# Performance work log

Measured on AMD Instinct MI355X. Metric: run time of the kernel, lower is better.

Reference implementation:

```python
import jax, jax.numpy as jnp
import numpy as np
from jax import lax

B, T, S, F = 16, 32, 128, 3
H = 256          # encoder_hidden = decoder_hidden = decoder_input
NH = 8           # n_head
TP = 4           # t_predict
DK = H // NH


def _lin(k, fan_in, shape):
    return jax.random.normal(k, shape, jnp.float32) * (1.0 / np.sqrt(fan_in))


def setup_inputs() -> dict:
    key = jax.random.key(0)
    ks = jax.random.split(key, 14)
    return {
        "input_data": jax.random.normal(ks[0], (B, T, S, F), jnp.float32),
        # encoder attention-LSTM cell (input_size=3)
        "enc_Wq": _lin(ks[1], H, (H, H)),
        "enc_Wk": _lin(ks[2], H, (H, H)),
        "enc_Wv": _lin(ks[3], H, (H, H)),
        "enc_Wg": _lin(ks[4], F + 2 * H, (F + 2 * H, 4 * H)),
        "enc_bg": jnp.zeros((4 * H,), jnp.float32),
        # decoder attention-LSTM cell (input_size=decoder_input=H)
        "dec_Wq": _lin(ks[5], H, (H, H)),
        "dec_Wk": _lin(ks[6], H, (H, H)),
        "dec_Wv": _lin(ks[7], H, (H, H)),
        "dec_Wg": _lin(ks[8], 3 * H, (3 * H, 4 * H)),
        "dec_bg": jnp.zeros((4 * H,), jnp.float32),
        # embedding Linear(encoder_hidden -> decoder_input)
        "emb_W": _lin(ks[9], H, (H, H)),
        "emb_b": jnp.zeros((H,), jnp.float32),
        # output Linear(decoder_hidden -> output_size=1)
        "out_W": _lin(ks[10], H, (H, 1)),
        "out_b": jnp.zeros((1,), jnp.float32),
    }


def spatial_hidden(h):
    # h: [B,S,H] -> [B,S,4,H] neighbors at offsets (+2,+1,-1,-2), zero-padded
    z1 = jnp.zeros_like(h[:, :1])
    z2 = jnp.zeros_like(h[:, :2])
    after1 = jnp.concatenate([h[:, 1:], z1], axis=1)
    before1 = jnp.concatenate([z1, h[:, :-1]], axis=1)
    after2 = jnp.concatenate([h[:, 2:], z2], axis=1)
    before2 = jnp.concatenate([z2, h[:, :-2]], axis=1)
    return jnp.stack([after2, after1, before1, before2], axis=2)


def attn_lstm_cell(x, h, c, sp, Wq, Wk, Wv, Wg, bg):
    # x:[B,S,Fin] h,c:[B,S,H] sp:[B,S,4,H]
    b, s, _ = h.shape
    q = (h @ Wq).reshape(b, s, NH, DK)
    k = (sp @ Wk).reshape(b, s, 4, NH, DK)
    v = (sp @ Wv).reshape(b, s, 4, NH, DK)
    scores = jnp.einsum('bshd,bsnhd->bshn', q, k) / np.sqrt(DK).astype(np.float32)
    attn = jax.nn.softmax(scores, axis=-1)
    ctx = jnp.einsum('bshn,bsnhd->bshd', attn, v).reshape(b, s, H)
    z = jnp.concatenate([x, h, ctx], axis=-1) @ Wg + bg
    i, f, g, o = jnp.split(z, 4, axis=-1)
    c_new = jax.nn.sigmoid(f) * c + jax.nn.sigmoid(i) * jnp.tanh(g)
    h_new = jax.nn.sigmoid(o) * jnp.tanh(c_new)
    return h_new, c_new


def reference(input_data, enc_Wq, enc_Wk, enc_Wv, enc_Wg, enc_bg,
              dec_Wq, dec_Wk, dec_Wv, dec_Wg, dec_bg,
              emb_W, emb_b, out_W, out_b):
    b, t, s, f = input_data.shape
    eh = jnp.zeros((b, s, H), input_data.dtype)
    ec = jnp.zeros((b, s, H), input_data.dtype)
    dh = jnp.zeros((b, s, H), input_data.dtype)

    cur = jnp.swapaxes(input_data[:, :-1], 0, 1)  # [T-1,B,S,F]
    nxt = jnp.swapaxes(input_data[:, 1:], 0, 1)   # [T-1,B,S,F]

    def step(carry, xt):
        eh, ec, dh = carry
        x_cur, x_nxt = xt
        esp = spatial_hidden(eh)
        dsp = spatial_hidden(dh)
        eh, ec = attn_lstm_cell(x_cur, eh, ec, esp, enc_Wq, enc_Wk, enc_Wv, enc_Wg, enc_bg)
        code = jax.nn.sigmoid(eh @ emb_W + emb_b)
        # NOTE: original code passes decoder_h as both h and c (decoder_c unused)
        dh, _ = attn_lstm_cell(code, dh, dh, dsp, dec_Wq, dec_Wk, dec_Wv, dec_Wg, dec_bg)
        out = dh @ out_W + out_b                                   # [B,S,1]
        In = jnp.concatenate([x_nxt[:, 0:1, 1:2], out[:, :-1, :]], axis=1)
        num = x_cur[:, :, 2:3] + In - out
        next_data = jnp.concatenate([out, In, num], axis=2)        # [B,S,3]
        return (eh, ec, dh), next_data

    _, outs = lax.scan(step, (eh, ec, dh), (cur, nxt))
    # keep only steps with time >= t_predict
    return jnp.swapaxes(outs[TP:], 0, 1)  # [B, T-TP-1, S, 3]
```

## Files before the change

kernel.cpp:

```cpp
#include <hip/hip_runtime.h>
#include <hip/hip_bf16.h>

#define Bz 16
#define Tz 32
#define Sz 128
#define TPz 4
#define Mz (Bz*Sz)
#define NSTEP (Tz-1)

typedef __bf16 bf16x8 __attribute__((ext_vector_type(8)));
typedef float  f32x4  __attribute__((ext_vector_type(4)));

#define MFMA __builtin_amdgcn_mfma_f32_16x16x32_bf16

__device__ __forceinline__ float sigf(float x) { return 1.f/(1.f + __expf(-x)); }

__global__ __launch_bounds__(256) void prep3(
    const float* __restrict__ encWq, const float* __restrict__ encWk,
    const float* __restrict__ encWv, const float* __restrict__ encWg,
    const float* __restrict__ decWq, const float* __restrict__ decWk,
    const float* __restrict__ decWv, const float* __restrict__ decWg,
    const float* __restrict__ embW,
    __bf16* __restrict__ Pqkv_e, __bf16* __restrict__ Pqkv_d,
    __bf16* __restrict__ Pemb,   __bf16* __restrict__ Pg_e,
    __bf16* __restrict__ Pg_d)
{
    int id = blockIdx.x * 256 + threadIdx.x;
    if (id < 768*256) {
        int f = id >> 9, e = id & 511, l = e >> 3, j = e & 7;
        int nt = f >> 3, kt = f & 7;
        int n = nt*16 + (l & 15), k = kt*32 + (l >> 4)*8 + j;
        float v = (n < 256) ? encWq[k*256 + n]
                : (n < 512) ? encWk[k*256 + (n-256)]
                            : encWv[k*256 + (n-512)];
        Pqkv_e[id] = (__bf16)v; return;
    }
    id -= 768*256;
    if (id < 768*256) {
        int f = id >> 9, e = id & 511, l = e >> 3, j = e & 7;
        int nt = f >> 3, kt = f & 7;
        int n = nt*16 + (l & 15), k = kt*32 + (l >> 4)*8 + j;
        float v = (n < 256) ? decWq[k*256 + n]
                : (n < 512) ? decWk[k*256 + (n-256)]
                            : decWv[k*256 + (n-512)];
        Pqkv_d[id] = (__bf16)v; return;
    }
    id -= 768*256;
    if (id < 256*256) {
        int f = id >> 9, e = id & 511, l = e >> 3, j = e & 7;
        int nt = f >> 3, kt = f & 7;
        int n = nt*16 + (l & 15), k = kt*32 + (l >> 4)*8 + j;
        Pemb[id] = (__bf16)embW[k*256 + n]; return;
    }
    id -= 256*256;
    if (id < 1024*512) {
        int f = id >> 9, e = id & 511, l = e >> 3, j = e & 7;
        int nt = f >> 4, kt = f & 15;
        int cht = nt >> 2, g = nt & 3;
        int ch = cht*16 + (l & 15), k = kt*32 + (l >> 4)*8 + j;
        Pg_e[id] = (__bf16)encWg[(size_t)(3 + k)*1024 + g*256 + ch]; return;
    }
    id -= 1024*512;
    if (id < 1024*768) {
        int f = id >> 9, e = id & 511, l = e >> 3, j = e & 7;
        int nt = f / 24, kt = f % 24;
        int cht = nt >> 2, g = nt & 3;
        int ch = cht*16 + (l & 15), k = kt*32 + (l >> 4)*8 + j;
        Pg_d[id] = (__bf16)decWg[(size_t)k*1024 + g*256 + ch]; return;
    }
}

__device__ __forceinline__ void qkv_lds(
    const __bf16* src264, const __bf16* __restrict__ P,
    __bf16* qL, __bf16* kvL, int tid)
{
    const int w = tid >> 6, lane = tid & 63, quad = (lane >> 4), lr = lane & 15;
    #pragma unroll
    for (int ng = 0; ng < 3; ++ng) {
        const int ntA = w*6 + ng*2;
        f32x4 acc[2][3];
        #pragma unroll
        for (int i = 0; i < 2; ++i)
            #pragma unroll
            for (int m = 0; m < 3; ++m) acc[i][m] = f32x4{0.f,0.f,0.f,0.f};
        for (int kt = 0; kt < 8; ++kt) {
            bf16x8 a0 = *(const bf16x8*)&src264[(lr)*264      + kt*32 + quad*8];
            bf16x8 a1 = *(const bf16x8*)&src264[(16 + lr)*264 + kt*32 + quad*8];
            bf16x8 a2 = *(const bf16x8*)&src264[(32 + lr)*264 + kt*32 + quad*8];
            bf16x8 b0 = *(const bf16x8*)&P[((size_t)(ntA*8 + kt)*64 + lane)*8];
            bf16x8 b1 = *(const bf16x8*)&P[((size_t)((ntA+1)*8 + kt)*64 + lane)*8];
            acc[0][0] = MFMA(a0, b0, acc[0][0], 0,0,0);
            acc[0][1] = MFMA(a1, b0, acc[0][1], 0,0,0);
            acc[0][2] = MFMA(a2, b0, acc[0][2], 0,0,0);
            acc[1][0] = MFMA(a0, b1, acc[1][0], 0,0,0);
            acc[1][1] = MFMA(a1, b1, acc[1][1], 0,0,0);
            acc[1][2] = MFMA(a2, b1, acc[1][2], 0,0,0);
        }
        #pragma unroll
        for (int i = 0; i < 2; ++i) {
            const int col = (ntA + i)*16 + lr;
            #pragma unroll
            for (int m = 0; m < 3; ++m)
                #pragma unroll
                for (int r = 0; r < 4; ++r) {
                    const int row = m*16 + quad*4 + r;
                    const float v = acc[i][m][r];
                    if (col < 256) {
                        if (row >= 2 && row < 34) qL[(row-2)*264 + col] = (__bf16)v;
                    } else if (row < 36) {
                        kvL[row*520 + (col - 256)] = (__bf16)v;
                    }
                }
        }
    }
}

__device__ __forceinline__ void attn_lds(
    const __bf16* qL, const __bf16* kvL, __bf16* cxL, int s0, int tid)
{
    const int w = tid >> 6, lane = tid & 63, quad = lane >> 4, lr = lane & 15;
    const int r = 4*w + quad, s = s0 + r, ch0 = lr*16;

    float q[16];
    {
        bf16x8 q0 = *(const bf16x8*)&qL[r*264 + ch0];
        bf16x8 q1 = *(const bf16x8*)&qL[r*264 + ch0 + 8];
        #pragma unroll
        for (int i = 0; i < 8; ++i) { q[i] = (float)q0[i]; q[8+i] = (float)q1[i]; }
    }
    bf16x8 zv;
    #pragma unroll
    for (int i = 0; i < 8; ++i) zv[i] = (__bf16)0.f;

    const int offs[4] = {2, 1, -1, -2};
    float sc[4]; bf16x8 v0[4], v1[4];
    #pragma unroll
    for (int n = 0; n < 4; ++n) {
        const int s2 = s + offs[n];
        const bool ok = ((unsigned)s2 < 128u);
        const int lrow = r + offs[n] + 2;
        float p = 0.f;
        if (ok) {
            bf16x8 k0 = *(const bf16x8*)&kvL[lrow*520 + ch0];
            bf16x8 k1 = *(const bf16x8*)&kvL[lrow*520 + ch0 + 8];
            v0[n] = *(const bf16x8*)&kvL[lrow*520 + 256 + ch0];
            v1[n] = *(const bf16x8*)&kvL[lrow*520 + 256 + ch0 + 8];
            #pragma unroll
            for (int i = 0; i < 8; ++i) p += q[i]*(float)k0[i] + q[8+i]*(float)k1[i];
        } else { v0[n] = zv; v1[n] = zv; }
        p += __shfl_xor(p, 1);
        sc[n] = ok ? p * 0.17677669529663687f : 0.f;
    }
    const float mx = fmaxf(fmaxf(sc[0], sc[1]), fmaxf(sc[2], sc[3]));
    float se = 0.f, aw[4];
    #pragma unroll
    for (int n = 0; n < 4; ++n) { aw[n] = __expf(sc[n] - mx); se += aw[n]; }
    const float inv = 1.f / se;
    float cx[16];
    #pragma unroll
    for (int i = 0; i < 16; ++i) cx[i] = 0.f;
    #pragma unroll
    for (int n = 0; n < 4; ++n)
        #pragma unroll
        for (int i = 0; i < 8; ++i) {
            cx[i]   += aw[n]*(float)v0[n][i];
            cx[8+i] += aw[n]*(float)v1[n][i];
        }
    bf16x8 o0, o1;
    #pragma unroll
    for (int i = 0; i < 8; ++i) { o0[i] = (__bf16)(cx[i]*inv); o1[i] = (__bf16)(cx[8+i]*inv); }
    *(bf16x8*)&cxL[r*264 + ch0]     = o0;
    *(bf16x8*)&cxL[r*264 + ch0 + 8] = o1;
}

#define SM_A264   0
#define SM_R      19008
#define SM_CODE   35904
#define SM_Q      56448
#define SM_MISC   73344
#define SM_TOTAL  73856

__global__ __launch_bounds__(512, 4) void step_k(
    int k, const float* __restrict__ input,
    __bf16* __restrict__ P, __bf16* __restrict__ Q,
    const __bf16* __restrict__ Pqkv_e, const __bf16* __restrict__ Pqkv_d,
    const __bf16* __restrict__ Pemb,   const __bf16* __restrict__ Pg_e,
    const __bf16* __restrict__ Pg_d,
    const float* __restrict__ encWg, const float* __restrict__ encbg,
    const float* __restrict__ decbg, const float* __restrict__ embb,
    const float* __restrict__ outW,
    float* __restrict__ ec, float* __restrict__ outbuf)
{
    __shared__ __attribute__((aligned(16))) char SM[SM_TOTAL];

    const int tid  = threadIdx.x;
    const int w    = tid >> 6;
    const int lane = tid & 63;
    const int quad = lane >> 4, lr = lane & 15;
    const int mt = w >> 2, ct = w & 3;

    __bf16* aL  = (__bf16*)(SM + SM_A264);
    __bf16* kvL = (__bf16*)(SM + SM_R);
    __bf16* qL  = (__bf16*)(SM + SM_Q);
    __bf16* cxL = qL;

    if (blockIdx.x >= 256) {
        if (k >= NSTEP) return;
        const int bid = blockIdx.x - 256;
        const int b = bid >> 4, rg = (bid >> 2) & 3, qt = bid & 3;
        const int gbatch = b*128, s0 = rg*32, grow0 = gbatch + s0;
        const int ch = qt*64 + ct*16 + lr;
        float* xL = (float*)(SM + SM_MISC);

        for (int v = tid; v < 36*32; v += 512) {
            const int row = v >> 5, seg = v & 31, s = s0 - 2 + row;
            bf16x8 val;
            if ((unsigned)s < 128u)
                val = *(const bf16x8*)&P[(size_t)(gbatch + s)*512 + seg*8];
            else {
                #pragma unroll
                for (int i = 0; i < 8; ++i) val[i] = (__bf16)0.f;
            }
            *(bf16x8*)&aL[row*264 + seg*8] = val;
        }
        if (tid < 96) xL[tid] = input[((size_t)(b*Tz + k)*Sz + s0)*3 + tid];
        __syncthreads();

        qkv_lds(aL, Pqkv_e, qL, kvL, tid);
        __syncthreads();
        attn_lds(qL, kvL, cxL, s0, tid);
        __syncthreads();

        float wx0[4], wx1[4], wx2[4], bgv[4];
        #pragma unroll
        for (int g = 0; g < 4; ++g) {
            const int c = g*256 + ch;
            wx0[g] = encWg[c]; wx1[g] = encWg[1024 + c]; wx2[g] = encWg[2048 + c];
            bgv[g] = encbg[c];
        }
        f32x4 acc[4];
        #pragma unroll
        for (int g = 0; g < 4; ++g) acc[g] = f32x4{0.f,0.f,0.f,0.f};
        for (int kt = 0; kt < 16; ++kt) {
            const __bf16* As = (kt < 8)
                ? &aL [(2 + mt*16 + lr)*264 + kt*32 + quad*8]
                : &cxL[(mt*16 + lr)*264 + (kt-8)*32 + quad*8];
            bf16x8 af = *(const bf16x8*)As;
            #pragma unroll
            for (int g = 0; g < 4; ++g) {
                const int nt = qt*16 + ct*4 + g;
                bf16x8 bf = *(const bf16x8*)&Pg_e[((size_t)(nt*16 + kt)*64 + lane)*8];
                acc[g] = MFMA(af, bf, acc[g], 0,0,0);
            }
        }
        #pragma unroll
        for (int r = 0; r < 4; ++r) {
            const int row = mt*16 + quad*4 + r;
            const float x0 = xL[row*3], x1 = xL[row*3+1], x2 = xL[row*3+2];
            const float zi = acc[0][r] + x0*wx0[0] + x1*wx1[0] + x2*wx2[0] + bgv[0];
            const float zf = acc[1][r] + x0*wx0[1] + x1*wx1[1] + x2*wx2[1] + bgv[1];
            const float zg = acc[2][r] + x0*wx0[2] + x1*wx1[2] + x2*wx2[2] + bgv[2];
            const float zo = acc[3][r] + x0*wx0[3] + x1*wx1[3] + x2*wx2[3] + bgv[3];
            const size_t ei = (size_t)(grow0 + row)*256 + ch;
            const float cn = sigf(zf)*ec[ei] + sigf(zi)*tanhf(zg);
            ec[ei] = cn;
            Q[(size_t)(grow0 + row)*512 + ch] = (__bf16)(sigf(zo)*tanhf(cn));
        }
    } else {
        if (k < 1) return;
        const int td = k - 1;
        const int bid = blockIdx.x;
        const int b = bid >> 4, rg = (bid >> 2) & 3, qt = bid & 3;
        const int gbatch = b*128, s0 = rg*32, grow0 = gbatch + s0;
        const int ch = qt*64 + ct*16 + lr;
        __bf16* dhL   = aL;
        __bf16* ehtL  = (__bf16*)(SM + SM_R);
        __bf16* codeL = (__bf16*)(SM + SM_CODE);
        float* outredL = (float*)(SM + SM_MISC);

        for (int v = tid; v < 32*32; v += 512) {
            const int row = v >> 5, seg = v & 31;
            *(bf16x8*)&ehtL[row*264 + seg*8] =
                *(const bf16x8*)&P[(size_t)(grow0 + row)*512 + seg*8];
        }
        for (int v = tid; v < 36*32; v += 512) {
            const int row = v >> 5, seg = v & 31, s = s0 - 2 + row;
            bf16x8 val;
            if ((unsigned)s < 128u)
                val = *(const bf16x8*)&Q[(size_t)(gbatch + s)*512 + 256 + seg*8];
            else {
                #pragma unroll
                for (int i = 0; i < 8; ++i) val[i] = (__bf16)0.f;
            }
            *(bf16x8*)&dhL[row*264 + seg*8] = val;
        }
        __syncthreads();

        {
            f32x4 cacc[2][2];
            #pragma unroll
            for (int m = 0; m < 2; ++m)
                #pragma unroll
                for (int i = 0; i < 2; ++i) cacc[m][i] = f32x4{0.f,0.f,0.f,0.f};
            for (int kt = 0; kt < 8; ++kt) {
                bf16x8 a0 = *(const bf16x8*)&ehtL[(lr)*264      + kt*32 + quad*8];
                bf16x8 a1 = *(const bf16x8*)&ehtL[(16 + lr)*264 + kt*32 + quad*8];
                #pragma unroll
                for (int i = 0; i < 2; ++i) {
                    bf16x8 bf = *(const bf16x8*)&Pemb[((size_t)((2*w + i)*8 + kt)*64 + lane)*8];
                    cacc[0][i] = MFMA(a0, bf, cacc[0][i], 0,0,0);
                    cacc[1][i] = MFMA(a1, bf, cacc[1][i], 0,0,0);
                }
            }
            __syncthreads();
            #pragma unroll
            for (int i = 0; i < 2; ++i) {
                const int col = (2*w + i)*16 + lr;
                const float bb = embb[col];
                #pragma unroll
                for (int m = 0; m < 2; ++m)
                    #pragma unroll
                    for (int r = 0; r < 4; ++r)
                        codeL[(m*16 + quad*4 + r)*264 + col] = (__bf16)sigf(cacc[m][i][r] + bb);
            }
        }
        __syncthreads();

        float bgv[4];
        #pragma unroll
        for (int g = 0; g < 4; ++g) bgv[g] = decbg[g*256 + ch];
        const float ow = outW[ch];

        f32x4 acc[4];
        #pragma unroll
        for (int g = 0; g < 4; ++g) acc[g] = f32x4{0.f,0.f,0.f,0.f};
        for (int kt = 0; kt < 8; ++kt) {
            bf16x8 af = *(const bf16x8*)&codeL[(mt*16 + lr)*264 + kt*32 + quad*8];
            #pragma unroll
            for (int g = 0; g < 4; ++g) {
                const int nt = qt*16 + ct*4 + g;
                bf16x8 bf = *(const bf16x8*)&Pg_d[((size_t)(nt*24 + kt)*64 + lane)*8];
                acc[g] = MFMA(af, bf, acc[g], 0,0,0);
            }
        }
        __syncthreads();

        qkv_lds(dhL, Pqkv_d, qL, kvL, tid);
        __syncthreads();
        attn_lds(qL, kvL, cxL, s0, tid);
        __syncthreads();

        for (int kt = 8; kt < 24; ++kt) {
            const __bf16* As = (kt < 16)
                ? &dhL[(2 + mt*16 + lr)*264 + (kt-8)*32 + quad*8]
                : &cxL[(mt*16 + lr)*264 + (kt-16)*32 + quad*8];
            bf16x8 af = *(const bf16x8*)As;
            #pragma unroll
            for (int g = 0; g < 4; ++g) {
                const int nt = qt*16 + ct*4 + g;
                bf16x8 bf = *(const bf16x8*)&Pg_d[((size_t)(nt*24 + kt)*64 + lane)*8];
                acc[g] = MFMA(af, bf, acc[g], 0,0,0);
            }
        }
        #pragma unroll
        for (int r = 0; r < 4; ++r) {
            const int row = mt*16 + quad*4 + r;
            const float zi = acc[0][r] + bgv[0];
            const float zf = acc[1][r] + bgv[1];
            const float zg = acc[2][r] + bgv[2];
            const float zo = acc[3][r] + bgv[3];
            const float c_old = (float)dhL[(2 + row)*264 + ch];
            const float cn = sigf(zf)*c_old + sigf(zi)*tanhf(zg);
            const float h  = sigf(zo)*tanhf(cn);
            P[(size_t)(grow0 + row)*512 + 256 + ch] = (__bf16)h;
            float pv = h * ow;
            pv += __shfl_xor(pv, 1); pv += __shfl_xor(pv, 2);
            pv += __shfl_xor(pv, 4); pv += __shfl_xor(pv, 8);
            if (lr == 0) outredL[row*4 + ct] = pv;
        }
        __syncthreads();
        if (tid < 32) {
            const float s4 = outredL[tid*4] + outredL[tid*4+1]
                           + outredL[tid*4+2] + outredL[tid*4+3];
            atomicAdd(&outbuf[(size_t)td*Mz + grow0 + tid], s4);
        }
    }
}

__global__ __launch_bounds__(256) void assemble_k(
    const float* __restrict__ outbuf, const float* __restrict__ input,
    const float* __restrict__ outb, float* __restrict__ out)
{
    const int idx = blockIdx.x*256 + threadIdx.x;
    const int NT = NSTEP - TPz;
    if (idx >= Bz*NT*Sz) return;
    const int s  = idx & 127;
    const int bi = idx >> 7;
    const int i  = bi % NT;
    const int b  = bi / NT;
    const int t  = i + TPz;
    const float ob = outb[0];
    const float o  = outbuf[t*Mz + (b<<7) + s] + ob;
    const float In = (s == 0)
        ? input[((size_t)(b*Tz + t + 1)*Sz)*3 + 1]
        : outbuf[t*Mz + (b<<7) + s - 1] + ob;
    const float num = input[((size_t)(b*Tz + t)*Sz + s)*3 + 2] + In - o;
    const size_t base = ((size_t)(b*NT + i)*Sz + s)*3;
    out[base+0] = o;
    out[base+1] = In;
    out[base+2] = num;
}

extern "C" void kernel_launch(void* const* d_in, const int* in_sizes, int n_in,
                              void* d_out, int out_size, void* d_ws, size_t ws_size,
                              hipStream_t stream)
{
    const float* input = (const float*)d_in[0];
    const float* encWq = (const float*)d_in[1];
    const float* encWk = (const float*)d_in[2];
    const float* encWv = (const float*)d_in[3];
    const float* encWg = (const float*)d_in[4];
    const float* encbg = (const float*)d_in[5];
    const float* decWq = (const float*)d_in[6];
    const float* decWk = (const float*)d_in[7];
    const float* decWv = (const float*)d_in[8];
    const float* decWg = (const float*)d_in[9];
    const float* decbg = (const float*)d_in[10];
    const float* embW  = (const float*)d_in[11];
    const float* embb  = (const float*)d_in[12];
    const float* outW  = (const float*)d_in[13];
    const float* outb  = (const float*)d_in[14];

    char* ws = (char*)d_ws;
    size_t off = 0;
    auto alloc = [&](size_t bytes) -> void* {
        void* p = ws + off;
        off += (bytes + 255) & ~(size_t)255;
        return p;
    };
    __bf16* Pqkv_e = (__bf16*)alloc((size_t)768*256*2);
    __bf16* Pqkv_d = (__bf16*)alloc((size_t)768*256*2);
    __bf16* Pemb   = (__bf16*)alloc((size_t)256*256*2);
    __bf16* Pg_e   = (__bf16*)alloc((size_t)1024*512*2);
    __bf16* Pg_d   = (__bf16*)alloc((size_t)1024*768*2);
    __bf16* Xa     = (__bf16*)alloc((size_t)Mz*512*2);
    __bf16* Xb     = (__bf16*)alloc((size_t)Mz*512*2);
    float*  ec     = (float*) alloc((size_t)Mz*256*4);
    float*  outbuf = (float*) alloc((size_t)NSTEP*Mz*4);

    hipMemsetAsync(Xa, 0, (size_t)Mz*512*2, stream);
    hipMemsetAsync(ec, 0, (size_t)Mz*256*4, stream);
    hipMemsetAsync(outbuf, 0, (size_t)NSTEP*Mz*4, stream);

    prep3<<<6912, 256, 0, stream>>>(encWq, encWk, encWv, encWg,
                                    decWq, decWk, decWv, decWg, embW,
                                    Pqkv_e, Pqkv_d, Pemb, Pg_e, Pg_d);

    for (int k = 0; k <= NSTEP; ++k) {
        __bf16* P = (k & 1) ? Xb : Xa;
        __bf16* Q = (k & 1) ? Xa : Xb;
        step_k<<<512, 512, 0, stream>>>(k, input, P, Q,
                                        Pqkv_e, Pqkv_d, Pemb, Pg_e, Pg_d,
                                        encWg, encbg, decbg, embb, outW,
                                        ec, outbuf);
    }
    assemble_k<<<(Bz*(NSTEP-TPz)*Sz + 255)/256, 256, 0, stream>>>(
        outbuf, input, outb, (float*)d_out);
}
```

Baseline: 1.276 ms.

## Fuse per-step launches into a persistent kernel with neighbor progress flags

Replaces the 32 per-timestep kernel launches with one persistent kernel in which each block loops over all steps. Blocks wait on atomic progress counters of only the neighboring encoder and decoder tiles they depend on, instead of a full grid-wide launch boundary. State reads use relaxed agent-scope atomic loads so that fresh data is seen. It removes launch overhead and global barriers, but it depends on all 512 blocks being co-resident and adds spin-wait cost, with a guard that could silently break on timeout.

Result: slower. 5.094 ms (+299.2%).

```diff
diff --git a/kernel.cpp b/kernel.cpp
--- a/kernel.cpp
+++ b/kernel.cpp
@@ -14,6 +14,15 @@
 #define MFMA __builtin_amdgcn_mfma_f32_16x16x32_bf16
 
 __device__ __forceinline__ float sigf(float x) { return 1.f/(1.f + __expf(-x)); }
+
+__device__ __forceinline__ bf16x8 ld_state16(const __bf16* p) {
+    unsigned long long* q = (unsigned long long*)p;
+    unsigned long long lo = __hip_atomic_load(q,     __ATOMIC_RELAXED, __HIP_MEMORY_SCOPE_AGENT);
+    unsigned long long hi = __hip_atomic_load(q + 1, __ATOMIC_RELAXED, __HIP_MEMORY_SCOPE_AGENT);
+    union { unsigned long long u[2]; bf16x8 v; } x;
+    x.u[0] = lo; x.u[1] = hi;
+    return x.v;
+}
 
 __global__ __launch_bounds__(256) void prep3(
     const float* __restrict__ encWq, const float* __restrict__ encWk,
@@ -180,16 +189,17 @@
 #define SM_MISC   73344
 #define SM_TOTAL  73856
 
-__global__ __launch_bounds__(512, 4) void step_k(
-    int k, const float* __restrict__ input,
-    __bf16* __restrict__ P, __bf16* __restrict__ Q,
+__global__ __launch_bounds__(512, 4) void fused_scan(
+    const float* __restrict__ input,
+    __bf16* __restrict__ Xa, __bf16* __restrict__ Xb,
     const __bf16* __restrict__ Pqkv_e, const __bf16* __restrict__ Pqkv_d,
     const __bf16* __restrict__ Pemb,   const __bf16* __restrict__ Pg_e,
     const __bf16* __restrict__ Pg_d,
     const float* __restrict__ encWg, const float* __restrict__ encbg,
     const float* __restrict__ decbg, const float* __restrict__ embb,
     const float* __restrict__ outW,
-    float* __restrict__ ec, float* __restrict__ outbuf)
+    float* __restrict__ ec, float* __restrict__ outbuf,
+    int* __restrict__ encProg, int* __restrict__ decProg)
 {
     __shared__ __attribute__((aligned(16))) char SM[SM_TOTAL];
 
@@ -199,191 +209,232 @@
     const int quad = lane >> 4, lr = lane & 15;
     const int mt = w >> 2, ct = w & 3;
 
+    const bool isEnc = (blockIdx.x >= 256);
+    const int bid = isEnc ? ((int)blockIdx.x - 256) : (int)blockIdx.x;
+    const int b = bid >> 4, rg = (bid >> 2) & 3, qt = bid & 3;
+    const int gbatch = b*128, s0 = rg*32, grow0 = gbatch + s0;
+    const int ch = qt*64 + ct*16 + lr;
+
     __bf16* aL  = (__bf16*)(SM + SM_A264);
     __bf16* kvL = (__bf16*)(SM + SM_R);
     __bf16* qL  = (__bf16*)(SM + SM_Q);
     __bf16* cxL = qL;
 
-    if (blockIdx.x >= 256) {
-        if (k >= NSTEP) return;
-        const int bid = blockIdx.x - 256;
-        const int b = bid >> 4, rg = (bid >> 2) & 3, qt = bid & 3;
-        const int gbatch = b*128, s0 = rg*32, grow0 = gbatch + s0;
-        const int ch = qt*64 + ct*16 + lr;
-        float* xL = (float*)(SM + SM_MISC);
-
-        for (int v = tid; v < 36*32; v += 512) {
-            const int row = v >> 5, seg = v & 31, s = s0 - 2 + row;
-            bf16x8 val;
-            if ((unsigned)s < 128u)
-                val = *(const bf16x8*)&P[(size_t)(gbatch + s)*512 + seg*8];
-            else {
+    int* prodPtr = nullptr; int off = 0;
+    if (isEnc) {
+        if (tid < 12) {
+            const int rr = rg - 1 + (tid >> 2), qq = tid & 3;
+            if (rr >= 0 && rr < 4) { prodPtr = &encProg[b*16 + rr*4 + qq]; off = 0; }
+        } else if (tid < 16) {
+            prodPtr = &decProg[b*16 + rg*4 + (tid - 12)]; off = -1;
+        }
+    } else {
+        if (tid < 4) {
+            prodPtr = &encProg[b*16 + rg*4 + tid]; off = 1;
+        } else if (tid < 16) {
+            const int j = tid - 4;
+            const int rr = rg - 1 + (j >> 2), qq = j & 3;
+            if (rr >= 0 && rr < 4) { prodPtr = &decProg[b*16 + rr*4 + qq]; off = 0; }
+        }
+    }
+    int* myFlag = isEnc ? &encProg[bid] : &decProg[bid];
+
+    for (int step = 0; step < NSTEP; ++step) {
+        if (prodPtr) {
+            const int target = step + off;
+            if (target > 0) {
+                int guard = 0;
+                while (__hip_atomic_load(prodPtr, __ATOMIC_RELAXED,
+                                         __HIP_MEMORY_SCOPE_AGENT) < target) {
+                    __builtin_amdgcn_s_sleep(2);
+                    if (++guard > (1 << 20)) break;
+                }
+            }
+        }
+        asm volatile("" ::: "memory");
+        __syncthreads();
+
+        const int kd = isEnc ? step : (step + 1);
+        __bf16* P = (kd & 1) ? Xb : Xa;
+        __bf16* Q = (kd & 1) ? Xa : Xb;
+
+        if (isEnc) {
+            const int k = step;
+            float* xL = (float*)(SM + SM_MISC);
+
+            for (int v = tid; v < 36*32; v += 512) {
+                const int row = v >> 5, seg = v & 31, s = s0 - 2 + row;
+                bf16x8 val;
+                if ((unsigned)s < 128u)
+                    val = ld_state16(&P[(size_t)(gbatch + s)*512 + seg*8]);
+                else {
+                    #pragma unroll
+                    for (int i = 0; i < 8; ++i) val[i] = (__bf16)0.f;
+                }
+                *(bf16x8*)&aL[row*264 + seg*8] = val;
+            }
+            if (tid < 96) xL[tid] = input[((size_t)(b*Tz + k)*Sz + s0)*3 + tid];
+            __syncthreads();
+
+            qkv_lds(aL, Pqkv_e, qL, kvL, tid);
+            __syncthreads();
+            attn_lds(qL, kvL, cxL, s0, tid);
+            __syncthreads();
+
+            float wx0[4], wx1[4], wx2[4], bgv[4];
+            #pragma unroll
+            for (int g = 0; g < 4; ++g) {
+                const int c = g*256 + ch;
+                wx0[g] = encWg[c]; wx1[g] = encWg[1024 + c]; wx2[g] = encWg[2048 + c];
+                bgv[g] = encbg[c];
+            }
+            f32x4 acc[4];
+            #pragma unroll
+            for (int g = 0; g < 4; ++g) acc[g] = f32x4{0.f,0.f,0.f,0.f};
+            for (int kt = 0; kt < 16; ++kt) {
+                const __bf16* As = (kt < 8)
+                    ? &aL [(2 + mt*16 + lr)*264 + kt*32 + quad*8]
+                    : &cxL[(mt*16 + lr)*264 + (kt-8)*32 + quad*8];
+                bf16x8 af = *(const bf16x8*)As;
                 #pragma unroll
-                for (int i = 0; i < 8; ++i) val[i] = (__bf16)0.f;
-            }
-            *(bf16x8*)&aL[row*264 + seg*8] = val;
-        }
-        if (tid < 96) xL[tid] = input[((size_t)(b*Tz + k)*Sz + s0)*3 + tid];
-        __syncthreads();
-
-        qkv_lds(aL, Pqkv_e, qL, kvL, tid);
-        __syncthreads();
-        attn_lds(qL, kvL, cxL, s0, tid);
-        __syncthreads();
-
-        float wx0[4], wx1[4], wx2[4], bgv[4];
-        #pragma unroll
-        for (int g = 0; g < 4; ++g) {
-            const int c = g*256 + ch;
-            wx0[g] = encWg[c]; wx1[g] = encWg[1024 + c]; wx2[g] = encWg[2048 + c];
-            bgv[g] = encbg[c];
-        }
-        f32x4 acc[4];
-        #pragma unroll
-        for (int g = 0; g < 4; ++g) acc[g] = f32x4{0.f,0.f,0.f,0.f};
-        for (int kt = 0; kt < 16; ++kt) {
-            const __bf16* As = (kt < 8)
-                ? &aL [(2 + mt*16 + lr)*264 + kt*32 + quad*8]
-                : &cxL[(mt*16 + lr)*264 + (kt-8)*32 + quad*8];
-            bf16x8 af = *(const bf16x8*)As;
-            #pragma unroll
-            for (int g = 0; g < 4; ++g) {
-                const int nt = qt*16 + ct*4 + g;
-                bf16x8 bf = *(const bf16x8*)&Pg_e[((size_t)(nt*16 + kt)*64 + lane)*8];
-                acc[g] = MFMA(af, bf, acc[g], 0,0,0);
-            }
-        }
-        #pragma unroll
-        for (int r = 0; r < 4; ++r) {
-            const int row = mt*16 + quad*4 + r;
-            const float x0 = xL[row*3], x1 = xL[row*3+1], x2 = xL[row*3+2];
-            const float zi = acc[0][r] + x0*wx0[0] + x1*wx1[0] + x2*wx2[0] + bgv[0];
-            const float zf = acc[1][r] + x0*wx0[1] + x1*wx1[1] + x2*wx2[1] + bgv[1];
-            const float zg = acc[2][r] + x0*wx0[2] + x1*wx1[2] + x2*wx2[2] + bgv[2];
-            const float zo = acc[3][r] + x0*wx0[3] + x1*wx1[3] + x2*wx2[3] + bgv[3];
-            const size_t ei = (size_t)(grow0 + row)*256 + ch;
-            const float cn = sigf(zf)*ec[ei] + sigf(zi)*tanhf(zg);
-            ec[ei] = cn;
-            Q[(size_t)(grow0 + row)*512 + ch] = (__bf16)(sigf(zo)*tanhf(cn));
-        }
-    } else {
-        if (k < 1) return;
-        const int td = k - 1;
-        const int bid = blockIdx.x;
-        const int b = bid >> 4, rg = (bid >> 2) & 3, qt = bid & 3;
-        const int gbatch = b*128, s0 = rg*32, grow0 = gbatch + s0;
-        const int ch = qt*64 + ct*16 + lr;
-        __bf16* dhL   = aL;
-        __bf16* ehtL  = (__bf16*)(SM + SM_R);
-        __bf16* codeL = (__bf16*)(SM + SM_CODE);
-        float* outredL = (float*)(SM + SM_MISC);
-
-        for (int v = tid; v < 32*32; v += 512) {
-            const int row = v >> 5, seg = v & 31;
-            *(bf16x8*)&ehtL[row*264 + seg*8] =
-                *(const bf16x8*)&P[(size_t)(grow0 + row)*512 + seg*8];
-        }
-        for (int v = tid; v < 36*32; v += 512) {
-            const int row = v >> 5, seg = v & 31, s = s0 - 2 + row;
-            bf16x8 val;
-            if ((unsigned)s < 128u)
-                val = *(const bf16x8*)&Q[(size_t)(gbatch + s)*512 + 256 + seg*8];
-            else {
-                #pragma unroll
-                for (int i = 0; i < 8; ++i) val[i] = (__bf16)0.f;
-            }
-            *(bf16x8*)&dhL[row*264 + seg*8] = val;
-        }
-        __syncthreads();
-
-        {
-            f32x4 cacc[2][2];
-            #pragma unroll
-            for (int m = 0; m < 2; ++m)
-                #pragma unroll
-                for (int i = 0; i < 2; ++i) cacc[m][i] = f32x4{0.f,0.f,0.f,0.f};
-            for (int kt = 0; kt < 8; ++kt) {
-                bf16x8 a0 = *(const bf16x8*)&ehtL[(lr)*264      + kt*32 + quad*8];
-                bf16x8 a1 = *(const bf16x8*)&ehtL[(16 + lr)*264 + kt*32 + quad*8];
-                #pragma unroll
-                for (int i = 0; i < 2; ++i) {
-                    bf16x8 bf = *(const bf16x8*)&Pemb[((size_t)((2*w + i)*8 + kt)*64 + lane)*8];
-                    cacc[0][i] = MFMA(a0, bf, cacc[0][i], 0,0,0);
-                    cacc[1][i] = MFMA(a1, bf, cacc[1][i], 0,0,0);
-                }
-            }
-            __syncthreads();
-            #pragma unroll
-            for (int i = 0; i < 2; ++i) {
-                const int col = (2*w + i)*16 + lr;
-                const float bb = embb[col];
+                for (int g = 0; g < 4; ++g) {
+                    const int nt = qt*16 + ct*4 + g;
+                    bf16x8 bf = *(const bf16x8*)&Pg_e[((size_t)(nt*16 + kt)*64 + lane)*8];
+                    acc[g] = MFMA(af, bf, acc[g], 0,0,0);
+                }
+            }
+            #pragma unroll
+            for (int r = 0; r < 4; ++r) {
+                const int row = mt*16 + quad*4 + r;
+                const float x0 = xL[row*3], x1 = xL[row*3+1], x2 = xL[row*3+2];
+                const float zi = acc[0][r] + x0*wx0[0] + x1*wx1[0] + x2*wx2[0] + bgv[0];
+                const float zf = acc[1][r] + x0*wx0[1] + x1*wx1[1] + x2*wx2[1] + bgv[1];
+                const float zg = acc[2][r] + x0*wx0[2] + x1*wx1[2] + x2*wx2[2] + bgv[2];
+                const float zo = acc[3][r] + x0*wx0[3] + x1*wx1[3] + x2*wx2[3] + bgv[3];
+                const size_t ei = (size_t)(grow0 + row)*256 + ch;
+                const float cn = sigf(zf)*ec[ei] + sigf(zi)*tanhf(zg);
+                ec[ei] = cn;
+                Q[(size_t)(grow0 + row)*512 + ch] = (__bf16)(sigf(zo)*tanhf(cn));
+            }
+        } else {
+            const int td = step;
+            __bf16* dhL   = aL;
+            __bf16* ehtL  = (__bf16*)(SM + SM_R);
+            __bf16* codeL = (__bf16*)(SM + SM_CODE);
+            float* outredL = (float*)(SM + SM_MISC);
+
+            for (int v = tid; v < 32*32; v += 512) {
+                const int row = v >> 5, seg = v & 31;
+                *(bf16x8*)&ehtL[row*264 + seg*8] =
+                    ld_state16(&P[(size_t)(grow0 + row)*512 + seg*8]);
+            }
+            for (int v = tid; v < 36*32; v += 512) {
+                const int row = v >> 5, seg = v & 31, s = s0 - 2 + row;
+                bf16x8 val;
+                if ((unsigned)s < 128u)
+                    val = ld_state16(&Q[(size_t)(gbatch + s)*512 + 256 + seg*8]);
+                else {
+                    #pragma unroll
+                    for (int i = 0; i < 8; ++i) val[i] = (__bf16)0.f;
+                }
+                *(bf16x8*)&dhL[row*264 + seg*8] = val;
+            }
+            __syncthreads();
+
+            {
+                f32x4 cacc[2][2];
                 #pragma unroll
                 for (int m = 0; m < 2; ++m)
                     #pragma unroll
-                    for (int r = 0; r < 4; ++r)
-                        codeL[(m*16 + quad*4 + r)*264 + col] = (__bf16)sigf(cacc[m][i][r] + bb);
-            }
-        }
+                    for (int i = 0; i < 2; ++i) cacc[m][i] = f32x4{0.f,0.f,0.f,0.f};
+                for (int kt = 0; kt < 8; ++kt) {
+                    bf16x8 a0 = *(const bf16x8*)&ehtL[(lr)*264      + kt*32 + quad*8];
+                    bf16x8 a1 = *(const bf16x8*)&ehtL[(16 + lr)*264 + kt*32 + quad*8];
+                    #pragma unroll
+                    for (int i = 0; i < 2; ++i) {
+                        bf16x8 bf = *(const bf16x8*)&Pemb[((size_t)((2*w + i)*8 + kt)*64 + lane)*8];
+                        cacc[0][i] = MFMA(a0, bf, cacc[0][i], 0,0,0);
+                        cacc[1][i] = MFMA(a1, bf, cacc[1][i], 0,0,0);
+                    }
+                }
+                __syncthreads();
+                #pragma unroll
+                for (int i = 0; i < 2; ++i) {
+                    const int col = (2*w + i)*16 + lr;
+                    const float bb = embb[col];
+                    #pragma unroll
+                    for (int m = 0; m < 2; ++m)
+                        #pragma unroll
+                        for (int r = 0; r < 4; ++r)
+                            codeL[(m*16 + quad*4 + r)*264 + col] = (__bf16)sigf(cacc[m][i][r] + bb);
+                }
+            }
+            __syncthreads();
+
+            float bgv[4];
+            #pragma unroll
+            for (int g = 0; g < 4; ++g) bgv[g] = decbg[g*256 + ch];
+            const float ow = outW[ch];
+
+            f32x4 acc[4];
+            #pragma unroll
+            for (int g = 0; g < 4; ++g) acc[g] = f32x4{0.f,0.f,0.f,0.f};
+            for (int kt = 0; kt < 8; ++kt) {
+                bf16x8 af = *(const bf16x8*)&codeL[(mt*16 + lr)*264 + kt*32 + quad*8];
+                #pragma unroll
+                for (int g = 0; g < 4; ++g) {
+                    const int nt = qt*16 + ct*4 + g;
+                    bf16x8 bf = *(const bf16x8*)&Pg_d[((size_t)(nt*24 + kt)*64 + lane)*8];
+                    acc[g] = MFMA(af, bf, acc[g], 0,0,0);
+                }
+            }
+            __syncthreads();
+
+            qkv_lds(dhL, Pqkv_d, qL, kvL, tid);
+            __syncthreads();
+            attn_lds(qL, kvL, cxL, s0, tid);
+            __syncthreads();
+
+            for (int kt = 8; kt < 24; ++kt) {
+                const __bf16* As = (kt < 16)
+                    ? &dhL[(2 + mt*16 + lr)*264 + (kt-8)*32 + quad*8]
+                    : &cxL[(mt*16 + lr)*264 + (kt-16)*32 + quad*8];
+                bf16x8 af = *(const bf16x8*)As;
+                #pragma unroll
+                for (int g = 0; g < 4; ++g) {
+                    const int nt = qt*16 + ct*4 + g;
+                    bf16x8 bf = *(const bf16x8*)&Pg_d[((size_t)(nt*24 + kt)*64 + lane)*8];
+                    acc[g] = MFMA(af, bf, acc[g], 0,0,0);
+                }
+            }
+            #pragma unroll
+            for (int r = 0; r < 4; ++r) {
+                const int row = mt*16 + quad*4 + r;
+                const float zi = acc[0][r] + bgv[0];
+                const float zf = acc[1][r] + bgv[1];
+                const float zg = acc[2][r] + bgv[2];
+                const float zo = acc[3][r] + bgv[3];
+                const float c_old = (float)dhL[(2 + row)*264 + ch];
+                const float cn = sigf(zf)*c_old + sigf(zi)*tanhf(zg);
+                const float h  = sigf(zo)*tanhf(cn);
+                P[(size_t)(grow0 + row)*512 + 256 + ch] = (__bf16)h;
+                float pv = h * ow;
+                pv += __shfl_xor(pv, 1); pv += __shfl_xor(pv, 2);
+                pv += __shfl_xor(pv, 4); pv += __shfl_xor(pv, 8);
+                if (lr == 0) outredL[row*4 + ct] = pv;
+            }
+            __syncthreads();
+            if (tid < 32) {
+                const float s4 = outredL[tid*4] + outredL[tid*4+1]
+                               + outredL[tid*4+2] + outredL[tid*4+3];
+                atomicAdd(&outbuf[(size_t)td*Mz + grow0 + tid], s4);
+            }
+        }
+
         __syncthreads();
-
-        float bgv[4];
-        #pragma unroll
-        for (int g = 0; g < 4; ++g) bgv[g] = decbg[g*256 + ch];
-        const float ow = outW[ch];
-
-        f32x4 acc[4];
-        #pragma unroll
-        for (int g = 0; g < 4; ++g) acc[g] = f32x4{0.f,0.f,0.f,0.f};
-        for (int kt = 0; kt < 8; ++kt) {
-            bf16x8 af = *(const bf16x8*)&codeL[(mt*16 + lr)*264 + kt*32 + quad*8];
-            #pragma unroll
-            for (int g = 0; g < 4; ++g) {
-                const int nt = qt*16 + ct*4 + g;
-                bf16x8 bf = *(const bf16x8*)&Pg_d[((size_t)(nt*24 + kt)*64 + lane)*8];
-                acc[g] = MFMA(af, bf, acc[g], 0,0,0);
-            }
-        }
-        __syncthreads();
-
-        qkv_lds(dhL, Pqkv_d, qL, kvL, tid);
-        __syncthreads();
-        attn_lds(qL, kvL, cxL, s0, tid);
-        __syncthreads();
-
-        for (int kt = 8; kt < 24; ++kt) {
-            const __bf16* As = (kt < 16)
-                ? &dhL[(2 + mt*16 + lr)*264 + (kt-8)*32 + quad*8]
-                : &cxL[(mt*16 + lr)*264 + (kt-16)*32 + quad*8];
-            bf16x8 af = *(const bf16x8*)As;
-            #pragma unroll
-            for (int g = 0; g < 4; ++g) {
-                const int nt = qt*16 + ct*4 + g;
-                bf16x8 bf = *(const bf16x8*)&Pg_d[((size_t)(nt*24 + kt)*64 + lane)*8];
-                acc[g] = MFMA(af, bf, acc[g], 0,0,0);
-            }
-        }
-        #pragma unroll
-        for (int r = 0; r < 4; ++r) {
-            const int row = mt*16 + quad*4 + r;
-            const float zi = acc[0][r] + bgv[0];
-            const float zf = acc[1][r] + bgv[1];
-            const float zg = acc[2][r] + bgv[2];
-            const float zo = acc[3][r] + bgv[3];
-            const float c_old = (float)dhL[(2 + row)*264 + ch];
-            const float cn = sigf(zf)*c_old + sigf(zi)*tanhf(zg);
-            const float h  = sigf(zo)*tanhf(cn);
-            P[(size_t)(grow0 + row)*512 + 256 + ch] = (__bf16)h;
-            float pv = h * ow;
-            pv += __shfl_xor(pv, 1); pv += __shfl_xor(pv, 2);
-            pv += __shfl_xor(pv, 4); pv += __shfl_xor(pv, 8);
-            if (lr == 0) outredL[row*4 + ct] = pv;
-        }
-        __syncthreads();
-        if (tid < 32) {
-            const float s4 = outredL[tid*4] + outredL[tid*4+1]
-                           + outredL[tid*4+2] + outredL[tid*4+3];
-            atomicAdd(&outbuf[(size_t)td*Mz + grow0 + tid], s4);
-        }
+        if (tid == 0)
+            __hip_atomic_store(myFlag, step + 1, __ATOMIC_RELEASE,
+                               __HIP_MEMORY_SCOPE_AGENT);
     }
 }
 
@@ -447,23 +498,24 @@
     __bf16* Xb     = (__bf16*)alloc((size_t)Mz*512*2);
     float*  ec     = (float*) alloc((size_t)Mz*256*4);
     float*  outbuf = (float*) alloc((size_t)NSTEP*Mz*4);
+    int*    prog   = (int*)   alloc((size_t)512*4);
 
     hipMemsetAsync(Xa, 0, (size_t)Mz*512*2, stream);
     hipMemsetAsync(ec, 0, (size_t)Mz*256*4, stream);
     hipMemsetAsync(outbuf, 0, (size_t)NSTEP*Mz*4, stream);
+    hipMemsetAsync(prog, 0, (size_t)512*4, stream);
 
     prep3<<<6912, 256, 0, stream>>>(encWq, encWk, encWv, encWg,
                                     decWq, decWk, decWv, decWg, embW,
                                     Pqkv_e, Pqkv_d, Pemb, Pg_e, Pg_d);
 
-    for (int k = 0; k <= NSTEP; ++k) {
-        __bf16* P = (k & 1) ? Xb : Xa;
-        __bf16* Q = (k & 1) ? Xa : Xb;
-        step_k<<<512, 512, 0, stream>>>(k, input, P, Q,
+    fused_scan<<<512, 512, 0, stream>>>(input, Xa, Xb,
                                         Pqkv_e, Pqkv_d, Pemb, Pg_e, Pg_d,
                                         encWg, encbg, decbg, embb, outW,
-                                        ec, outbuf);
-    }
+                                        ec, outbuf,
+                                        prog + 256,
+                                        prog);
+
     assemble_k<<<(Bz*(NSTEP-TPz)*Sz + 255)/256, 256, 0, stream>>>(
         outbuf, input, outb, (float*)d_out);
 }
```
